# Kernel optimization log

Measured on AMD Instinct MI355X. Metric: run time of the kernel, lower is better.

Reference implementation:

```python
import jax, jax.numpy as jnp
import numpy as np

L = 2        # rnn_layers
H = 512      # hidden size
T_MAX = 20   # text_max_len
V = 10000    # NUM_WORDS
B = 32       # batch
S = 49       # spatial positions (7x7)


def setup_inputs() -> dict:
    key = jax.random.key(0)
    ks = jax.random.split(key, 12)
    w = lambda k, shape: jax.random.normal(k, shape, dtype=jnp.float32) * 0.02
    return {
        "img_channels": jax.random.normal(ks[0], (B, 512, 7, 7), dtype=jnp.float32),
        "pooled": jax.random.normal(ks[1], (B, H), dtype=jnp.float32),
        "embed_table": w(ks[2], (V, H)),
        "Wq": w(ks[3], (H, H)), "bq": jnp.zeros((H,), jnp.float32),
        "Wk": w(ks[4], (S, S)), "bk": jnp.zeros((S,), jnp.float32),
        "Wv": w(ks[5], (S, S)), "bv": jnp.zeros((S,), jnp.float32),
        "Wih": w(ks[6], (L, 4 * H, H)), "Whh": w(ks[7], (L, 4 * H, H)),
        "bih": jnp.zeros((L, 4 * H), jnp.float32), "bhh": jnp.zeros((L, 4 * H), jnp.float32),
        "projW": w(ks[8], (V, H)), "projb": jnp.zeros((V,), jnp.float32),
        "hattW": w(ks[9], (H, 2 * H)), "hattb": jnp.zeros((H,), jnp.float32),
        "sos_idx": 1,
    }


def _lstm_cell(x, h, c, wih, whh, bi, bh):
    # PyTorch gate order: i, f, g, o
    g = x @ wih.T + bi + h @ whh.T + bh
    i, f, gg, o = jnp.split(g, 4, axis=-1)
    c2 = jax.nn.sigmoid(f) * c + jax.nn.sigmoid(i) * jnp.tanh(gg)
    return jax.nn.sigmoid(o) * jnp.tanh(c2), c2


def reference(img_channels, pooled, embed_table, Wq, bq, Wk, bk, Wv, bv,
              Wih, Whh, bih, bhh, projW, projb, hattW, hattb, sos_idx):
    Bsz = img_channels.shape[0]
    chan = img_channels.reshape(Bsz, 512, -1)           # [B,512,49]
    # keys/values are step-invariant: precompute once
    keys = jnp.tanh(chan @ Wk.T + bk)                    # [B,512,49]
    values = jnp.tanh(chan @ Wv.T + bv)                  # [B,512,49]

    emb0 = jnp.broadcast_to(embed_table[sos_idx], (Bsz, H))   # <SOS> embedding
    h0 = jnp.broadcast_to(pooled[None], (L, Bsz, H))
    c0 = h0

    def step(carry, _):
        emb, h, c = carry
        x = emb
        hs, cs = [], []
        for l in range(L):  # small fixed layer count
            hl, cl = _lstm_cell(x, h[l], c[l], Wih[l], Whh[l], bih[l], bhh[l])
            hs.append(hl); cs.append(cl)
            x = hl
        out = x                                          # [B,H] top-layer output
        h = jnp.stack(hs); c = jnp.stack(cs)
        # greedy next-token embedding (no teacher forcing)
        logits = out @ projW.T + projb                   # [B,V]
        emb_next = embed_table[jnp.argmax(logits, axis=-1)]
        # cross-attention gated hidden update (all layers at once)
        q = jnp.tanh(h @ Wq.T + bq)                      # [L,B,H]
        scores = jnp.einsum('lbd,bds->lbs', q, keys) / 7.0
        w = jax.nn.softmax(scores, axis=-1)              # [L,B,49]
        attn = jnp.einsum('lbs,bds->lbd', w, values)     # [L,B,H]
        h = jnp.tanh(jnp.concatenate([attn, h], axis=-1) @ hattW.T + hattb)
        return (emb_next, h, c), out

    _, outs = jax.lax.scan(step, (emb0, h0, c0), None, length=T_MAX - 1)
    pred = jnp.concatenate([emb0[None], outs], axis=0)   # [T,B,H]
    res = jnp.einsum('tbd,vd->bvt', pred, projW) + projb[None, :, None]
    return res                                           # [B,V,T]
```

## Files before the change

kernel.cpp:

```cpp
#include <hip/hip_runtime.h>

namespace {

constexpr int B = 32, H = 512, L = 2, T = 20, V = 10000, S = 49;

__device__ __forceinline__ float sigf(float x) { return 1.0f / (1.0f + expf(-x)); }
__device__ __forceinline__ float dot4(float4 a, float4 b) {
  return a.x*b.x + a.y*b.y + a.z*b.z + a.w*b.w;
}

__global__ __launch_bounds__(256) void kv_kernel(
    const float* __restrict__ chan,
    const float* __restrict__ Wk, const float* __restrict__ bk,
    const float* __restrict__ Wv, const float* __restrict__ bv,
    float* __restrict__ keysT, float* __restrict__ valuesT) {
  __shared__ float ch[64][52];
  __shared__ float wk[49][52], wv[49][52];
  int b = blockIdx.x >> 3, dt = blockIdx.x & 7;
  int tid = threadIdx.x;
  for (int i = tid; i < 49 * 49; i += 256) {
    int s = i / 49, j = i % 49;
    wk[s][j] = Wk[i]; wv[s][j] = Wv[i];
  }
  for (int i = tid; i < 64 * 49; i += 256) {
    int d = i / 49, j = i % 49;
    ch[d][j] = chan[((size_t)b * 512 + dt * 64 + d) * S + j];
  }
  __syncthreads();
  int dl = tid >> 2, sq = tid & 3;
  for (int s = sq; s < S; s += 4) {
    float ak = bk[s], av = bv[s];
    for (int j = 0; j < 49; ++j) {
      float cv = ch[dl][j];
      ak += cv * wk[s][j];
      av += cv * wv[s][j];
    }
    int d = dt * 64 + dl;
    keysT[((size_t)b * S + s) * H + d] = tanhf(ak);
    valuesT[((size_t)b * S + s) * H + d] = tanhf(av);
  }
}

__global__ void init_kernel(const float* __restrict__ pooled,
                            const float* __restrict__ embed,
                            const int* __restrict__ sos,
                            float* __restrict__ emb, float* __restrict__ h,
                            float* __restrict__ c) {
  int idx = blockIdx.x * 256 + threadIdx.x;
  float p = pooled[idx & (B * H - 1)];
  h[idx] = p;
  c[idx] = p;
  if (idx < B * H) emb[idx] = embed[sos[0] * H + (idx & (H - 1))];
}

__global__ __launch_bounds__(256) void lstm_kernel(
    const float* __restrict__ x, const float* __restrict__ hprev,
    const float* __restrict__ cprev,
    const float* __restrict__ Wih, const float* __restrict__ Whh,
    const float* __restrict__ bih, const float* __restrict__ bhh,
    float* __restrict__ hout, float* __restrict__ cout) {
  __shared__ __align__(16) float smem[32 * 512];
  int tid = threadIdx.x;
  int hi = blockIdx.x;
  int ko = tid & 15, rr = (tid >> 4) & 3, bh = tid >> 6;

  {
    const float4* xg = (const float4*)x;
    float4* s4 = (float4*)smem;
    for (int i = tid; i < 4096; i += 256) s4[i] = xg[i];
  }
  __syncthreads();

  float acc[8];
#pragma unroll
  for (int j = 0; j < 8; ++j) acc[j] = 0.f;
  {
    const float* wrow = Wih + ((size_t)rr * H + hi) * H;
    float4 w[8];
#pragma unroll
    for (int kk = 0; kk < 8; ++kk) w[kk] = *(const float4*)&wrow[kk * 64 + ko * 4];
#pragma unroll
    for (int j = 0; j < 8; ++j) {
      const float* xb = smem + (bh * 8 + j) * 512;
#pragma unroll
      for (int kk = 0; kk < 8; ++kk)
        acc[j] += dot4(*(const float4*)&xb[kk * 64 + ko * 4], w[kk]);
    }
  }
  __syncthreads();
  {
    const float4* hg = (const float4*)hprev;
    float4* s4 = (float4*)smem;
    for (int i = tid; i < 4096; i += 256) s4[i] = hg[i];
  }
  __syncthreads();
  {
    const float* wrow = Whh + ((size_t)rr * H + hi) * H;
    float4 w[8];
#pragma unroll
    for (int kk = 0; kk < 8; ++kk) w[kk] = *(const float4*)&wrow[kk * 64 + ko * 4];
#pragma unroll
    for (int j = 0; j < 8; ++j) {
      const float* xb = smem + (bh * 8 + j) * 512;
#pragma unroll
      for (int kk = 0; kk < 8; ++kk)
        acc[j] += dot4(*(const float4*)&xb[kk * 64 + ko * 4], w[kk]);
    }
  }
  __syncthreads();

#pragma unroll
  for (int j = 0; j < 8; ++j) {
    acc[j] += __shfl_xor(acc[j], 1);
    acc[j] += __shfl_xor(acc[j], 2);
    acc[j] += __shfl_xor(acc[j], 4);
    acc[j] += __shfl_xor(acc[j], 8);
  }
  float* gbuf = smem;
  if (ko == 0) {
    float bias = bih[rr * H + hi] + bhh[rr * H + hi];
#pragma unroll
    for (int j = 0; j < 8; ++j) gbuf[rr * 32 + bh * 8 + j] = acc[j] + bias;
  }
  __syncthreads();
  if (tid < 32) {
    int b = tid;
    float gi = gbuf[b], gf = gbuf[32 + b], gg = gbuf[64 + b], go = gbuf[96 + b];
    float c2 = sigf(gf) * cprev[b * H + hi] + sigf(gi) * tanhf(gg);
    hout[b * H + hi] = sigf(go) * tanhf(c2);
    cout[b * H + hi] = c2;
  }
}

__global__ __launch_bounds__(256) void projq_kernel(
    const float* __restrict__ xin,
    const float* __restrict__ projW, const float* __restrict__ projb,
    float* __restrict__ logits, float* __restrict__ ocol, int direct, int tcol,
    const float* __restrict__ hmid_all, const float* __restrict__ Wq,
    const float* __restrict__ bq, float* __restrict__ q) {
  __shared__ __align__(16) float xs[32 * 512];
  int blk = blockIdx.x, tid = threadIdx.x;
  int ko = tid & 15, vl = tid >> 4;

  if (blk < 625) {
    {
      const float4* xg = (const float4*)xin;
      float4* s4 = (float4*)xs;
      for (int i = tid; i < 4096; i += 256) s4[i] = xg[i];
    }
    __syncthreads();
    int v = blk * 16 + vl;
    const float* wrow = projW + (size_t)v * H;
    float4 w[8];
#pragma unroll
    for (int kk = 0; kk < 8; ++kk) w[kk] = *(const float4*)&wrow[kk * 64 + ko * 4];
    float acc[32];
#pragma unroll
    for (int b = 0; b < 32; ++b) acc[b] = 0.f;
    for (int b = 0; b < 32; ++b) {
      const float* xb = xs + b * 512;
#pragma unroll
      for (int kk = 0; kk < 8; ++kk)
        acc[b] += dot4(*(const float4*)&xb[kk * 64 + ko * 4], w[kk]);
    }
#pragma unroll
    for (int b = 0; b < 32; ++b) {
      acc[b] += __shfl_xor(acc[b], 1);
      acc[b] += __shfl_xor(acc[b], 2);
      acc[b] += __shfl_xor(acc[b], 4);
      acc[b] += __shfl_xor(acc[b], 8);
    }
    if (ko == 0) {
      float bias = projb[v];
      for (int b = 0; b < 32; ++b) {
        float r = acc[b] + bias;
        logits[b * V + v] = r;
        if (direct) ocol[((size_t)b * V + v) * T + tcol] = r;
        else        ocol[b * V + v] = r;
      }
    }
  } else {
    int b2 = blk - 625;
    int lg = b2 & 1, jg = b2 >> 1;
    {
      const float4* xg = (const float4*)(hmid_all + lg * 32 * H);
      float4* s4 = (float4*)xs;
      for (int i = tid; i < 4096; i += 256) s4[i] = xg[i];
    }
    __syncthreads();
    int j = jg * 16 + vl;
    const float* wrow = Wq + (size_t)j * H;
    float4 w[8];
#pragma unroll
    for (int kk = 0; kk < 8; ++kk) w[kk] = *(const float4*)&wrow[kk * 64 + ko * 4];
    float acc[32];
#pragma unroll
    for (int b = 0; b < 32; ++b) acc[b] = 0.f;
    for (int b = 0; b < 32; ++b) {
      const float* xb = xs + b * 512;
#pragma unroll
      for (int kk = 0; kk < 8; ++kk)
        acc[b] += dot4(*(const float4*)&xb[kk * 64 + ko * 4], w[kk]);
    }
#pragma unroll
    for (int b = 0; b < 32; ++b) {
      acc[b] += __shfl_xor(acc[b], 1);
      acc[b] += __shfl_xor(acc[b], 2);
      acc[b] += __shfl_xor(acc[b], 4);
      acc[b] += __shfl_xor(acc[b], 8);
    }
    if (ko == 0) {
      float bias = bq[j];
      for (int b = 0; b < 32; ++b)
        q[(lg * 32 + b) * H + j] = tanhf(acc[b] + bias);
    }
  }
}

__global__ __launch_bounds__(256) void sattn_kernel(
    const float* __restrict__ q, const float* __restrict__ keysT,
    const float* __restrict__ valuesT, const float* __restrict__ hmid,
    float* __restrict__ cat) {
  __shared__ __align__(16) float qv[528];
  __shared__ float scl[64];
  __shared__ float wts[64];
  int lb = blockIdx.x, tid = threadIdx.x;
  int b = lb & 31;
  {
    int c0 = tid, c1 = tid + 256;
    qv[(c0 >> 7) * 132 + (c0 & 127)] = q[lb * H + c0];
    qv[(c1 >> 7) * 132 + (c1 & 127)] = q[lb * H + c1];
  }
  __syncthreads();
  int kq = tid & 3, sl = tid >> 2;
  float acc = 0.f;
  if (sl < S) {
    const float* kr = keysT + ((size_t)b * S + sl) * H + kq * 128;
    const float* qr = &qv[kq * 132];
    for (int k = 0; k < 128; k += 4)
      acc += dot4(*(const float4*)&qr[k], *(const float4*)&kr[k]);
  }
  acc += __shfl_xor(acc, 1);
  acc += __shfl_xor(acc, 2);
  if (kq == 0 && sl < S) scl[sl] = acc * (1.0f / 7.0f);
  __syncthreads();
  if (tid < 64) {
    float sc = (tid < S) ? scl[tid] : -3.4e38f;
    float m = sc;
    for (int o = 32; o > 0; o >>= 1) m = fmaxf(m, __shfl_xor(m, o));
    float e = (tid < S) ? expf(sc - m) : 0.f;
    float sum = e;
    for (int o = 32; o > 0; o >>= 1) sum += __shfl_xor(sum, o);
    if (tid < S) wts[tid] = e / sum;
  }
  __syncthreads();
  float acc0 = 0.f, acc1 = 0.f;
  for (int s = 0; s < S; ++s) {
    float w = wts[s];
    const float* vr = valuesT + ((size_t)b * S + s) * H;
    acc0 += w * vr[tid];
    acc1 += w * vr[tid + 256];
  }
  cat[lb * 1024 + tid] = acc0;
  cat[lb * 1024 + tid + 256] = acc1;
  cat[lb * 1024 + 512 + tid] = hmid[lb * H + tid];
  cat[lb * 1024 + 768 + tid] = hmid[lb * H + tid + 256];
}

__global__ __launch_bounds__(256) void hattarg_kernel(
    const float* __restrict__ cat, const float* __restrict__ hattW,
    const float* __restrict__ hattb, float* __restrict__ h,
    const float* __restrict__ logits, const float* __restrict__ embed,
    float* __restrict__ emb) {
  __shared__ __align__(16) float smem[16 * 1024];
  int blk = blockIdx.x, tid = threadIdx.x;
  if (blk < 128) {
    int lbg = blk & 3, jg = blk >> 2;
    {
      const float4* cg = (const float4*)(cat + lbg * 16 * 1024);
      float4* s4 = (float4*)smem;
      for (int i = tid; i < 4096; i += 256) s4[i] = cg[i];
    }
    __syncthreads();
    int ko = tid & 15, jl = tid >> 4;
    int j = jg * 16 + jl;
    const float* wrow = hattW + (size_t)j * 1024;
    float4 w[16];
#pragma unroll
    for (int kk = 0; kk < 16; ++kk) w[kk] = *(const float4*)&wrow[kk * 64 + ko * 4];
    float acc[16];
#pragma unroll
    for (int lb = 0; lb < 16; ++lb) acc[lb] = 0.f;
    for (int lb = 0; lb < 16; ++lb) {
      const float* cb = smem + lb * 1024;
#pragma unroll
      for (int kk = 0; kk < 16; ++kk)
        acc[lb] += dot4(*(const float4*)&cb[kk * 64 + ko * 4], w[kk]);
    }
#pragma unroll
    for (int lb = 0; lb < 16; ++lb) {
      acc[lb] += __shfl_xor(acc[lb], 1);
      acc[lb] += __shfl_xor(acc[lb], 2);
      acc[lb] += __shfl_xor(acc[lb], 4);
      acc[lb] += __shfl_xor(acc[lb], 8);
    }
    if (ko == 0) {
      float bias = hattb[j];
      for (int lb = 0; lb < 16; ++lb)
        h[(lbg * 16 + lb) * H + j] = tanhf(acc[lb] + bias);
    }
  } else {
    int b = blk - 128;
    float* sv = smem;
    int* si = (int*)(smem + 256);
    float best = -3.4e38f;
    int bi = 0x7fffffff;
    for (int it = 0; it < 10; ++it) {
      int v0 = it * 1024 + tid * 4;
      if (v0 < V) {
        float4 lv = *(const float4*)&logits[b * V + v0];
        if (lv.x > best) { best = lv.x; bi = v0; }
        if (lv.y > best) { best = lv.y; bi = v0 + 1; }
        if (lv.z > best) { best = lv.z; bi = v0 + 2; }
        if (lv.w > best) { best = lv.w; bi = v0 + 3; }
      }
    }
    sv[tid] = best; si[tid] = bi;
    __syncthreads();
    for (int st = 128; st > 0; st >>= 1) {
      if (tid < st) {
        float ov = sv[tid + st]; int oi = si[tid + st];
        if (ov > sv[tid] || (ov == sv[tid] && oi < si[tid])) { sv[tid] = ov; si[tid] = oi; }
      }
      __syncthreads();
    }
    int idx = si[0];
    for (int i = tid; i < H; i += 256) emb[b * H + i] = embed[(size_t)idx * H + i];
  }
}

__global__ __launch_bounds__(256) void finalize_kernel(
    const float* __restrict__ slog, float* __restrict__ outp) {
  int idx = blockIdx.x * 256 + threadIdx.x;
  float vals[T];
#pragma unroll
  for (int t = 0; t < T; ++t) vals[t] = slog[(size_t)t * (B * V) + idx];
#pragma unroll
  for (int t = 0; t < T; t += 4)
    *(float4*)&outp[(size_t)idx * T + t] =
        make_float4(vals[t], vals[t + 1], vals[t + 2], vals[t + 3]);
}

}

extern "C" void kernel_launch(void* const* d_in, const int* in_sizes, int n_in,
                              void* d_out, int out_size, void* d_ws, size_t ws_size,
                              hipStream_t stream) {
  const float* chan   = (const float*)d_in[0];
  const float* pooled = (const float*)d_in[1];
  const float* embed  = (const float*)d_in[2];
  const float* Wq     = (const float*)d_in[3];
  const float* bq     = (const float*)d_in[4];
  const float* Wk     = (const float*)d_in[5];
  const float* bk     = (const float*)d_in[6];
  const float* Wv     = (const float*)d_in[7];
  const float* bv     = (const float*)d_in[8];
  const float* Wih    = (const float*)d_in[9];
  const float* Whh    = (const float*)d_in[10];
  const float* bih    = (const float*)d_in[11];
  const float* bhh    = (const float*)d_in[12];
  const float* projW  = (const float*)d_in[13];
  const float* projb  = (const float*)d_in[14];
  const float* hattW  = (const float*)d_in[15];
  const float* hattb  = (const float*)d_in[16];
  const int*   sos    = (const int*)d_in[17];

  float* out = (float*)d_out;
  float* ws  = (float*)d_ws;

  float* keysT   = ws;
  float* valuesT = keysT + B * S * 512;
  float* emb     = valuesT + B * S * 512;
  float* h       = emb + B * H;
  float* c       = h + L * B * H;
  float* hmid    = c + L * B * H;
  float* cat     = hmid + L * B * H;
  float* q       = cat + L * B * 1024;
  float* logits  = q + L * B * H;
  float* slog    = logits + B * V;

  size_t base_floats = (size_t)(slog - ws);
  bool staged = ws_size >= (base_floats + (size_t)T * B * V) * sizeof(float);

  kv_kernel<<<256, 256, 0, stream>>>(chan, Wk, bk, Wv, bv, keysT, valuesT);
  init_kernel<<<(L * B * H) / 256, 256, 0, stream>>>(pooled, embed, sos, emb, h, c);
  {
    float* oc = staged ? slog : out;
    projq_kernel<<<625, 256, 0, stream>>>(emb, projW, projb, logits, oc,
                                          staged ? 0 : 1, 0,
                                          hmid, Wq, bq, q);
  }

  for (int t = 0; t < T - 1; ++t) {
    float* oc = staged ? (slog + (size_t)(t + 1) * B * V) : out;
    lstm_kernel<<<512, 256, 0, stream>>>(emb, h, c, Wih, Whh, bih, bhh, hmid, c);
    lstm_kernel<<<512, 256, 0, stream>>>(hmid, h + B * H, c + B * H,
                                         Wih + 4 * H * H, Whh + 4 * H * H,
                                         bih + 4 * H, bhh + 4 * H,
                                         hmid + B * H, c + B * H);
    projq_kernel<<<689, 256, 0, stream>>>(hmid + B * H, projW, projb, logits, oc,
                                          staged ? 0 : 1, t + 1,
                                          hmid, Wq, bq, q);
    sattn_kernel<<<L * B, 256, 0, stream>>>(q, keysT, valuesT, hmid, cat);
    hattarg_kernel<<<160, 256, 0, stream>>>(cat, hattW, hattb, h,
                                            logits, embed, emb);
  }

  if (staged) finalize_kernel<<<(B * V) / 256, 256, 0, stream>>>(slog, out);
}
```

Before: 1.984 ms.

## Replace per-step kernel launches with a single persistent kernel using grid barriers

Fuses the whole decode loop (kv precompute, init, LSTM layers, projection, query, attention, argmax, hidden update, finalize) into one persistent kernel of 256 blocks that synchronise through an atomic-counter grid barrier. This removes roughly a hundred kernel launches and their launch gaps, and regroups stages so argmax runs alongside attention. It relies on all 256 blocks being co-resident. The barrier has a spin-count escape that could silently break correctness if it times out, and the old multi-kernel path is kept only as a fallback when workspace is too small.

Result: slower. 6.021 ms (+203.5%).

```diff
diff --git a/kernel.cpp b/kernel.cpp
--- a/kernel.cpp
+++ b/kernel.cpp
@@ -3,11 +3,383 @@
 namespace {
 
 constexpr int B = 32, H = 512, L = 2, T = 20, V = 10000, S = 49;
+constexpr int NB = 256, NT = 512;
 
 __device__ __forceinline__ float sigf(float x) { return 1.0f / (1.0f + expf(-x)); }
 __device__ __forceinline__ float dot4(float4 a, float4 b) {
   return a.x*b.x + a.y*b.y + a.z*b.z + a.w*b.w;
 }
+
+struct KParams {
+  const float *chan, *pooled, *embed, *Wq, *bq, *Wk, *bk, *Wv, *bv,
+              *Wih, *Whh, *bih, *bhh, *projW, *projb, *hattW, *hattb;
+  const int* sos;
+  float* out;
+  float* ws;
+  int* cnt;
+};
+
+__device__ __forceinline__ void gsync(int* cnt, int target) {
+  __syncthreads();
+  if (threadIdx.x == 0) {
+    __threadfence();
+    atomicAdd(cnt, 1);
+    unsigned spins = 0;
+    while (atomicAdd(cnt, 0) < target) {
+      __builtin_amdgcn_s_sleep(8);
+      if (++spins > (1u << 20)) break;
+    }
+    __threadfence();
+  }
+  __syncthreads();
+}
+
+
+__device__ __forceinline__ void stage64k(const float* __restrict__ src,
+                                         float* smem, int tid) {
+  const float4* g = (const float4*)src;
+  float4* s4 = (float4*)smem;
+  for (int i = tid; i < 4096; i += NT) s4[i] = g[i];
+}
+
+__device__ __forceinline__ void lstm_do(
+    const float* __restrict__ x, const float* __restrict__ hp,
+    float* __restrict__ cp, const float* __restrict__ Wih,
+    const float* __restrict__ Whh, const float* __restrict__ bih,
+    const float* __restrict__ bhh, float* __restrict__ ho,
+    float* smem, int blk, int tid) {
+  int tl = tid & 255, hh = tid >> 8;
+  int ko = tl & 15, rr = (tl >> 4) & 3, bh = tl >> 6;
+  int hi = blk * 2 + hh;
+  stage64k(x, smem, tid);
+  __syncthreads();
+  float acc[8];
+#pragma unroll
+  for (int j = 0; j < 8; ++j) acc[j] = 0.f;
+  {
+    const float* wrow = Wih + ((size_t)rr * H + hi) * H;
+    float4 w[8];
+#pragma unroll
+    for (int kk = 0; kk < 8; ++kk) w[kk] = *(const float4*)&wrow[kk * 64 + ko * 4];
+#pragma unroll
+    for (int j = 0; j < 8; ++j) {
+      const float* xb = smem + (bh * 8 + j) * 512;
+#pragma unroll
+      for (int kk = 0; kk < 8; ++kk)
+        acc[j] += dot4(*(const float4*)&xb[kk * 64 + ko * 4], w[kk]);
+    }
+  }
+  __syncthreads();
+  stage64k(hp, smem, tid);
+  __syncthreads();
+  {
+    const float* wrow = Whh + ((size_t)rr * H + hi) * H;
+    float4 w[8];
+#pragma unroll
+    for (int kk = 0; kk < 8; ++kk) w[kk] = *(const float4*)&wrow[kk * 64 + ko * 4];
+#pragma unroll
+    for (int j = 0; j < 8; ++j) {
+      const float* xb = smem + (bh * 8 + j) * 512;
+#pragma unroll
+      for (int kk = 0; kk < 8; ++kk)
+        acc[j] += dot4(*(const float4*)&xb[kk * 64 + ko * 4], w[kk]);
+    }
+  }
+  __syncthreads();
+#pragma unroll
+  for (int j = 0; j < 8; ++j) {
+    acc[j] += __shfl_xor(acc[j], 1);
+    acc[j] += __shfl_xor(acc[j], 2);
+    acc[j] += __shfl_xor(acc[j], 4);
+    acc[j] += __shfl_xor(acc[j], 8);
+  }
+  float* gbuf = smem;
+  if (ko == 0) {
+    float bias = bih[rr * H + hi] + bhh[rr * H + hi];
+#pragma unroll
+    for (int j = 0; j < 8; ++j) gbuf[hh * 128 + rr * 32 + bh * 8 + j] = acc[j] + bias;
+  }
+  __syncthreads();
+  if (tid < 64) {
+    int hs = tid >> 5, b = tid & 31;
+    int hi2 = blk * 2 + hs;
+    const float* gb = gbuf + hs * 128;
+    float gi = gb[b], gf = gb[32 + b], gg = gb[64 + b], go = gb[96 + b];
+    float c2 = sigf(gf) * cp[b * H + hi2] + sigf(gi) * tanhf(gg);
+    ho[b * H + hi2] = sigf(go) * tanhf(c2);
+    cp[b * H + hi2] = c2;
+  }
+}
+
+__device__ __forceinline__ void proj_do(
+    const float* __restrict__ x, float* __restrict__ dst,
+    const float* __restrict__ projW, const float* __restrict__ projb,
+    float* smem, int blk, int tid) {
+  stage64k(x, smem, tid);
+  __syncthreads();
+  int ko = tid & 15, vl = tid >> 4;
+  for (int chunk = blk; chunk < 313; chunk += NB) {
+    int v = chunk * 32 + vl;
+    if (v < V) {
+      const float* wrow = projW + (size_t)v * H;
+      float4 w[8];
+#pragma unroll
+      for (int kk = 0; kk < 8; ++kk) w[kk] = *(const float4*)&wrow[kk * 64 + ko * 4];
+      float acc[32];
+#pragma unroll
+      for (int b = 0; b < 32; ++b) acc[b] = 0.f;
+      for (int b = 0; b < 32; ++b) {
+        const float* xb = smem + b * 512;
+#pragma unroll
+        for (int kk = 0; kk < 8; ++kk)
+          acc[b] += dot4(*(const float4*)&xb[kk * 64 + ko * 4], w[kk]);
+      }
+#pragma unroll
+      for (int b = 0; b < 32; ++b) {
+        acc[b] += __shfl_xor(acc[b], 1);
+        acc[b] += __shfl_xor(acc[b], 2);
+        acc[b] += __shfl_xor(acc[b], 4);
+        acc[b] += __shfl_xor(acc[b], 8);
+      }
+      if (ko == 0) {
+        float bias = projb[v];
+        for (int b = 0; b < 32; ++b) dst[(size_t)b * V + v] = acc[b] + bias;
+      }
+    }
+  }
+}
+
+__device__ __forceinline__ void q_do(
+    const float* __restrict__ hmid, const float* __restrict__ Wq,
+    const float* __restrict__ bq, float* __restrict__ q,
+    float* smem, int u, int tid) {
+  int lg = u & 1, jg = u >> 1;
+  __syncthreads();
+  stage64k(hmid + (size_t)lg * B * H, smem, tid);
+  __syncthreads();
+  int ko = tid & 15, jl = tid >> 4;
+  int j = jg * 32 + jl;
+  const float* wrow = Wq + (size_t)j * H;
+  float4 w[8];
+#pragma unroll
+  for (int kk = 0; kk < 8; ++kk) w[kk] = *(const float4*)&wrow[kk * 64 + ko * 4];
+  float acc[32];
+#pragma unroll
+  for (int b = 0; b < 32; ++b) acc[b] = 0.f;
+  for (int b = 0; b < 32; ++b) {
+    const float* xb = smem + b * 512;
+#pragma unroll
+    for (int kk = 0; kk < 8; ++kk)
+      acc[b] += dot4(*(const float4*)&xb[kk * 64 + ko * 4], w[kk]);
+  }
+#pragma unroll
+  for (int b = 0; b < 32; ++b) {
+    acc[b] += __shfl_xor(acc[b], 1);
+    acc[b] += __shfl_xor(acc[b], 2);
+    acc[b] += __shfl_xor(acc[b], 4);
+    acc[b] += __shfl_xor(acc[b], 8);
+  }
+  if (ko == 0) {
+    float bias = bq[j];
+    for (int b = 0; b < 32; ++b)
+      q[(size_t)(lg * 32 + b) * H + j] = tanhf(acc[b] + bias);
+  }
+}
+
+__device__ __forceinline__ void sattn_do(
+    const float* __restrict__ q, const float* __restrict__ keysT,
+    const float* __restrict__ valuesT, const float* __restrict__ hmid,
+    float* __restrict__ cat, float* smem, int lb, int tid) {
+  float* qv = smem;
+  float* scl = smem + 544;
+  float* wts = smem + 608;
+  int b = lb & 31;
+  qv[(tid >> 7) * 132 + (tid & 127)] = q[(size_t)lb * H + tid];
+  __syncthreads();
+  int kq = tid & 3, sl = tid >> 2;
+  float acc = 0.f;
+  if (sl < S) {
+    const float* kr = keysT + ((size_t)b * S + sl) * H + kq * 128;
+    const float* qr = &qv[kq * 132];
+    for (int k = 0; k < 128; k += 4)
+      acc += dot4(*(const float4*)&qr[k], *(const float4*)&kr[k]);
+  }
+  acc += __shfl_xor(acc, 1);
+  acc += __shfl_xor(acc, 2);
+  if (kq == 0 && sl < S) scl[sl] = acc * (1.0f / 7.0f);
+  __syncthreads();
+  if (tid < 64) {
+    float sc = (tid < S) ? scl[tid] : -3.4e38f;
+    float m = sc;
+    for (int o = 32; o > 0; o >>= 1) m = fmaxf(m, __shfl_xor(m, o));
+    float e = (tid < S) ? expf(sc - m) : 0.f;
+    float sum = e;
+    for (int o = 32; o > 0; o >>= 1) sum += __shfl_xor(sum, o);
+    if (tid < S) wts[tid] = e / sum;
+  }
+  __syncthreads();
+  float a0 = 0.f;
+  for (int s = 0; s < S; ++s)
+    a0 += wts[s] * valuesT[((size_t)b * S + s) * H + tid];
+  cat[(size_t)lb * 1024 + tid] = a0;
+  cat[(size_t)lb * 1024 + 512 + tid] = hmid[(size_t)lb * H + tid];
+}
+
+__device__ __forceinline__ void argmax_do(
+    const float* __restrict__ lgts, const float* __restrict__ embed,
+    float* __restrict__ emb, float* smem, int b, int tid) {
+  float* sv = smem;
+  int* si = (int*)(smem + 512);
+  float best = -3.4e38f;
+  int bi = 0x7fffffff;
+  for (int it = 0; it < 5; ++it) {
+    int v0 = it * 2048 + tid * 4;
+    if (v0 < V) {
+      float4 lv = *(const float4*)&lgts[(size_t)b * V + v0];
+      if (lv.x > best) { best = lv.x; bi = v0; }
+      if (lv.y > best) { best = lv.y; bi = v0 + 1; }
+      if (lv.z > best) { best = lv.z; bi = v0 + 2; }
+      if (lv.w > best) { best = lv.w; bi = v0 + 3; }
+    }
+  }
+  sv[tid] = best; si[tid] = bi;
+  __syncthreads();
+  for (int st = 256; st > 0; st >>= 1) {
+    if (tid < st) {
+      float ov = sv[tid + st]; int oi = si[tid + st];
+      if (ov > sv[tid] || (ov == sv[tid] && oi < si[tid])) { sv[tid] = ov; si[tid] = oi; }
+    }
+    __syncthreads();
+  }
+  int idx = si[0];
+  emb[(size_t)b * H + tid] = embed[(size_t)idx * H + tid];
+}
+
+__device__ __forceinline__ void hatt_do(
+    const float* __restrict__ cat, const float* __restrict__ hattW,
+    const float* __restrict__ hattb, float* __restrict__ h,
+    float* smem, int blk, int tid) {
+  int lbg = blk & 3, jg = blk >> 2;
+  stage64k(cat + (size_t)lbg * 16 * 1024, smem, tid);
+  __syncthreads();
+  int ko = tid & 15, jl = tid >> 4;
+  int j = jg * 32 + jl;
+  const float* wrow = hattW + (size_t)j * 1024;
+  float4 w[16];
+#pragma unroll
+  for (int kk = 0; kk < 16; ++kk) w[kk] = *(const float4*)&wrow[kk * 64 + ko * 4];
+  float acc[16];
+#pragma unroll
+  for (int lb = 0; lb < 16; ++lb) acc[lb] = 0.f;
+  for (int lb = 0; lb < 16; ++lb) {
+    const float* cb = smem + lb * 1024;
+#pragma unroll
+    for (int kk = 0; kk < 16; ++kk)
+      acc[lb] += dot4(*(const float4*)&cb[kk * 64 + ko * 4], w[kk]);
+  }
+#pragma unroll
+  for (int lb = 0; lb < 16; ++lb) {
+    acc[lb] += __shfl_xor(acc[lb], 1);
+    acc[lb] += __shfl_xor(acc[lb], 2);
+    acc[lb] += __shfl_xor(acc[lb], 4);
+    acc[lb] += __shfl_xor(acc[lb], 8);
+  }
+  if (ko == 0) {
+    float bias = hattb[j];
+    for (int lb = 0; lb < 16; ++lb)
+      h[(size_t)(lbg * 16 + lb) * H + j] = tanhf(acc[lb] + bias);
+  }
+}
+
+__global__ __launch_bounds__(NT, 4) void persist(KParams p) {
+  __shared__ __align__(16) float smem[16384];
+  const int blk = blockIdx.x, tid = threadIdx.x;
+  int* cnt = p.cnt;
+  int ep = 0;
+
+  float* keysT   = p.ws;
+  float* valuesT = keysT + B * S * H;
+  float* emb     = valuesT + B * S * H;
+  float* h       = emb + B * H;
+  float* c       = h + L * B * H;
+  float* hmid    = c + L * B * H;
+  float* cat     = hmid + L * B * H;
+  float* q       = cat + L * B * 1024;
+  float* logits  = q + L * B * H;
+  float* slog    = logits + B * V;
+
+  {
+    float* ch = smem;
+    float* wk = smem + 64 * 52;
+    float* wv = wk + 49 * 52;
+    int b = blk >> 3, dt = blk & 7;
+    for (int i = tid; i < 49 * 49; i += NT) {
+      int s = i / 49, j = i % 49;
+      wk[s * 52 + j] = p.Wk[i]; wv[s * 52 + j] = p.Wv[i];
+    }
+    for (int i = tid; i < 64 * 49; i += NT) {
+      int d = i / 49, j = i % 49;
+      ch[d * 52 + j] = p.chan[((size_t)b * 512 + dt * 64 + d) * S + j];
+    }
+    __syncthreads();
+    int dl = tid >> 3, sq = tid & 7;
+    for (int s = sq; s < S; s += 8) {
+      float ak = p.bk[s], av = p.bv[s];
+      for (int j = 0; j < 49; ++j) {
+        float cv = ch[dl * 52 + j];
+        ak += cv * wk[s * 52 + j];
+        av += cv * wv[s * 52 + j];
+      }
+      int d = dt * 64 + dl;
+      keysT[((size_t)b * S + s) * H + d] = tanhf(ak);
+      valuesT[((size_t)b * S + s) * H + d] = tanhf(av);
+    }
+    int idx = blk * NT + tid;
+    if (idx < L * B * H) {
+      float pv = p.pooled[idx & (B * H - 1)];
+      h[idx] = pv; c[idx] = pv;
+      if (idx < B * H) emb[idx] = p.embed[(size_t)p.sos[0] * H + (idx & (H - 1))];
+    }
+  }
+  gsync(cnt, (++ep) * NB);
+
+  proj_do(emb, slog, p.projW, p.projb, smem, blk, tid);
+  gsync(cnt, (++ep) * NB);
+
+#pragma unroll 1
+  for (int t = 0; t < T - 1; ++t) {
+    lstm_do(emb, h, c, p.Wih, p.Whh, p.bih, p.bhh, hmid, smem, blk, tid);
+    gsync(cnt, (++ep) * NB);
+    lstm_do(hmid, h + B * H, c + B * H, p.Wih + 4 * H * H, p.Whh + 4 * H * H,
+            p.bih + 4 * H, p.bhh + 4 * H, hmid + B * H, smem, blk, tid);
+    gsync(cnt, (++ep) * NB);
+    proj_do(hmid + B * H, slog + (size_t)(t + 1) * B * V, p.projW, p.projb,
+            smem, blk, tid);
+    if (t < T - 2 && blk >= 57 && blk < 89)
+      q_do(hmid, p.Wq, p.bq, q, smem, blk - 57, tid);
+    gsync(cnt, (++ep) * NB);
+    if (t < T - 2) {
+      if (blk < 64)
+        sattn_do(q, keysT, valuesT, hmid, cat, smem, blk, tid);
+      else if (blk < 96)
+        argmax_do(slog + (size_t)(t + 1) * B * V, p.embed, emb, smem, blk - 64, tid);
+      gsync(cnt, (++ep) * NB);
+      if (blk < 64) hatt_do(cat, p.hattW, p.hattb, h, smem, blk, tid);
+      gsync(cnt, (++ep) * NB);
+    }
+  }
+
+  for (int i = blk * NT + tid; i < B * V; i += NB * NT) {
+    float vals[T];
+#pragma unroll
+    for (int t = 0; t < T; ++t) vals[t] = slog[(size_t)t * (B * V) + i];
+#pragma unroll
+    for (int t = 0; t < T; t += 4)
+      *(float4*)&p.out[(size_t)i * T + t] =
+          make_float4(vals[t], vals[t + 1], vals[t + 2], vals[t + 3]);
+  }
+}
+
 
 __global__ __launch_bounds__(256) void kv_kernel(
     const float* __restrict__ chan,
@@ -63,14 +435,12 @@
   int tid = threadIdx.x;
   int hi = blockIdx.x;
   int ko = tid & 15, rr = (tid >> 4) & 3, bh = tid >> 6;
-
   {
     const float4* xg = (const float4*)x;
     float4* s4 = (float4*)smem;
     for (int i = tid; i < 4096; i += 256) s4[i] = xg[i];
   }
   __syncthreads();
-
   float acc[8];
 #pragma unroll
   for (int j = 0; j < 8; ++j) acc[j] = 0.f;
@@ -108,7 +478,6 @@
     }
   }
   __syncthreads();
-
 #pragma unroll
   for (int j = 0; j < 8; ++j) {
     acc[j] += __shfl_xor(acc[j], 1);
@@ -141,7 +510,6 @@
   __shared__ __align__(16) float xs[32 * 512];
   int blk = blockIdx.x, tid = threadIdx.x;
   int ko = tid & 15, vl = tid >> 4;
-
   if (blk < 625) {
     {
       const float4* xg = (const float4*)xin;
@@ -277,9 +645,9 @@
   if (blk < 128) {
     int lbg = blk & 3, jg = blk >> 2;
     {
-      const float4* cg = (const float4*)(cat + lbg * 16 * 1024);
+      const float4* cg2 = (const float4*)(cat + lbg * 16 * 1024);
       float4* s4 = (float4*)smem;
-      for (int i = tid; i < 4096; i += 256) s4[i] = cg[i];
+      for (int i = tid; i < 4096; i += 256) s4[i] = cg2[i];
     }
     __syncthreads();
     int ko = tid & 15, jl = tid >> 4;
@@ -356,6 +724,7 @@
 extern "C" void kernel_launch(void* const* d_in, const int* in_sizes, int n_in,
                               void* d_out, int out_size, void* d_ws, size_t ws_size,
                               hipStream_t stream) {
+  (void)in_sizes; (void)n_in; (void)out_size;
   const float* chan   = (const float*)d_in[0];
   const float* pooled = (const float*)d_in[1];
   const float* embed  = (const float*)d_in[2];
@@ -376,7 +745,8 @@
   const int*   sos    = (const int*)d_in[17];
 
   float* out = (float*)d_out;
-  float* ws  = (float*)d_ws;
+  int*   cnt = (int*)d_ws;
+  float* ws  = (float*)d_ws + 64;
 
   float* keysT   = ws;
   float* valuesT = keysT + B * S * 512;
@@ -389,7 +759,19 @@
   float* logits  = q + L * B * H;
   float* slog    = logits + B * V;
 
-  size_t base_floats = (size_t)(slog - ws);
+  size_t need_floats = 64 + (size_t)(slog - ws) + (size_t)T * B * V;
+  bool fits = ws_size >= need_floats * sizeof(float);
+
+  if (fits) {
+    hipMemsetAsync(d_ws, 0, 256, stream);
+    KParams p = {chan, pooled, embed, Wq, bq, Wk, bk, Wv, bv,
+                 Wih, Whh, bih, bhh, projW, projb, hattW, hattb,
+                 sos, out, ws, cnt};
+    persist<<<NB, NT, 0, stream>>>(p);
+    return;
+  }
+
+  size_t base_floats = (size_t)(slog - ws) + 64;
   bool staged = ws_size >= (base_floats + (size_t)T * B * V) * sizeof(float);
 
   kv_kernel<<<256, 256, 0, stream>>>(chan, Wk, bk, Wv, bv, keysT, valuesT);
@@ -400,7 +782,6 @@
                                           staged ? 0 : 1, 0,
                                           hmid, Wq, bq, q);
   }
-
   for (int t = 0; t < T - 1; ++t) {
     float* oc = staged ? (slog + (size_t)(t + 1) * B * V) : out;
     lstm_kernel<<<512, 256, 0, stream>>>(emb, h, c, Wih, Whh, bih, bhh, hmid, c);
@@ -415,6 +796,5 @@
     hattarg_kernel<<<160, 256, 0, stream>>>(cat, hattW, hattb, h,
                                             logits, embed, emb);
   }
-
   if (staged) finalize_kernel<<<(B * V) / 256, 256, 0, stream>>>(slog, out);
 }
```

## Fuse setup kernels, merge query projection into attention, drop redundant final-step work

Applied to the files above, without the earlier changes.

When the staging workspace is available, this adds a single setup kernel that builds keys/values, initial states and the step-0 logits. The step-0 projection is computed once for the shared SOS embedding and broadcast across the batch. A new projsat kernel computes the vocab projection into the staged slice and lets each attention block compute its own query row before doing attention, which removes a separate launch. The argmax now reads from the staged logits, and the last step skips the attention and hidden-update work whose results are never used. Together these cut launches and redundant compute. The cost is that each attention block recomputes a full 512x512 GEMV row-set serially, so the query step loses parallelism.

Result: slower. 2.035 ms (+2.6%).

```diff
diff --git a/kernel.cpp b/kernel.cpp
--- a/kernel.cpp
+++ b/kernel.cpp
@@ -8,6 +8,344 @@
 __device__ __forceinline__ float dot4(float4 a, float4 b) {
   return a.x*b.x + a.y*b.y + a.z*b.z + a.w*b.w;
 }
+
+__global__ __launch_bounds__(256) void setup_kernel(
+    const float* __restrict__ chan,
+    const float* __restrict__ Wk, const float* __restrict__ bk,
+    const float* __restrict__ Wv, const float* __restrict__ bv,
+    float* __restrict__ keysT, float* __restrict__ valuesT,
+    const float* __restrict__ pooled, const float* __restrict__ embed,
+    const int* __restrict__ sos,
+    float* __restrict__ emb, float* __restrict__ h, float* __restrict__ c,
+    const float* __restrict__ projW, const float* __restrict__ projb,
+    float* __restrict__ slog0) {
+  __shared__ __align__(16) float smem[8448];
+  int blk = blockIdx.x, tid = threadIdx.x;
+  if (blk < 256) {
+    float* ch = smem;
+    float* wk = smem + 64 * 52;
+    float* wv = wk + 49 * 52;
+    int b = blk >> 3, dt = blk & 7;
+    for (int i = tid; i < 49 * 49; i += 256) {
+      int s = i / 49, j = i % 49;
+      wk[s * 52 + j] = Wk[i]; wv[s * 52 + j] = Wv[i];
+    }
+    for (int i = tid; i < 64 * 49; i += 256) {
+      int d = i / 49, j = i % 49;
+      ch[d * 52 + j] = chan[((size_t)b * 512 + dt * 64 + d) * S + j];
+    }
+    __syncthreads();
+    int dl = tid >> 2, sq = tid & 3;
+    for (int s = sq; s < S; s += 4) {
+      float ak = bk[s], av = bv[s];
+      for (int j = 0; j < 49; ++j) {
+        float cv = ch[dl * 52 + j];
+        ak += cv * wk[s * 52 + j];
+        av += cv * wv[s * 52 + j];
+      }
+      int d = dt * 64 + dl;
+      keysT[((size_t)b * S + s) * H + d] = tanhf(ak);
+      valuesT[((size_t)b * S + s) * H + d] = tanhf(av);
+    }
+  } else if (blk < 384) {
+    int idx = (blk - 256) * 256 + tid;
+    float p = pooled[idx & (B * H - 1)];
+    h[idx] = p;
+    c[idx] = p;
+    if (idx < B * H) emb[idx] = embed[(size_t)sos[0] * H + (idx & (H - 1))];
+  } else {
+    float* es = smem;
+    es[tid] = embed[(size_t)sos[0] * H + tid];
+    es[tid + 256] = embed[(size_t)sos[0] * H + tid + 256];
+    __syncthreads();
+    int ko = tid & 15, vl = tid >> 4;
+    int v = (blk - 384) * 16 + vl;
+    const float* wrow = projW + (size_t)v * H;
+    float4 w[8];
+#pragma unroll
+    for (int kk = 0; kk < 8; ++kk) w[kk] = *(const float4*)&wrow[kk * 64 + ko * 4];
+    float acc = 0.f;
+#pragma unroll
+    for (int kk = 0; kk < 8; ++kk)
+      acc += dot4(*(const float4*)&es[kk * 64 + ko * 4], w[kk]);
+    acc += __shfl_xor(acc, 1);
+    acc += __shfl_xor(acc, 2);
+    acc += __shfl_xor(acc, 4);
+    acc += __shfl_xor(acc, 8);
+    if (ko == 0) {
+      float r = acc + projb[v];
+      for (int b = 0; b < 32; ++b) slog0[(size_t)b * V + v] = r;
+    }
+  }
+}
+
+__global__ __launch_bounds__(256) void lstm_kernel(
+    const float* __restrict__ x, const float* __restrict__ hprev,
+    const float* __restrict__ cprev,
+    const float* __restrict__ Wih, const float* __restrict__ Whh,
+    const float* __restrict__ bih, const float* __restrict__ bhh,
+    float* __restrict__ hout, float* __restrict__ cout) {
+  __shared__ __align__(16) float smem[32 * 512];
+  int tid = threadIdx.x;
+  int hi = blockIdx.x;
+  int ko = tid & 15, rr = (tid >> 4) & 3, bh = tid >> 6;
+  {
+    const float4* xg = (const float4*)x;
+    float4* s4 = (float4*)smem;
+    for (int i = tid; i < 4096; i += 256) s4[i] = xg[i];
+  }
+  __syncthreads();
+  float acc[8];
+#pragma unroll
+  for (int j = 0; j < 8; ++j) acc[j] = 0.f;
+  {
+    const float* wrow = Wih + ((size_t)rr * H + hi) * H;
+    float4 w[8];
+#pragma unroll
+    for (int kk = 0; kk < 8; ++kk) w[kk] = *(const float4*)&wrow[kk * 64 + ko * 4];
+#pragma unroll
+    for (int j = 0; j < 8; ++j) {
+      const float* xb = smem + (bh * 8 + j) * 512;
+#pragma unroll
+      for (int kk = 0; kk < 8; ++kk)
+        acc[j] += dot4(*(const float4*)&xb[kk * 64 + ko * 4], w[kk]);
+    }
+  }
+  __syncthreads();
+  {
+    const float4* hg = (const float4*)hprev;
+    float4* s4 = (float4*)smem;
+    for (int i = tid; i < 4096; i += 256) s4[i] = hg[i];
+  }
+  __syncthreads();
+  {
+    const float* wrow = Whh + ((size_t)rr * H + hi) * H;
+    float4 w[8];
+#pragma unroll
+    for (int kk = 0; kk < 8; ++kk) w[kk] = *(const float4*)&wrow[kk * 64 + ko * 4];
+#pragma unroll
+    for (int j = 0; j < 8; ++j) {
+      const float* xb = smem + (bh * 8 + j) * 512;
+#pragma unroll
+      for (int kk = 0; kk < 8; ++kk)
+        acc[j] += dot4(*(const float4*)&xb[kk * 64 + ko * 4], w[kk]);
+    }
+  }
+  __syncthreads();
+#pragma unroll
+  for (int j = 0; j < 8; ++j) {
+    acc[j] += __shfl_xor(acc[j], 1);
+    acc[j] += __shfl_xor(acc[j], 2);
+    acc[j] += __shfl_xor(acc[j], 4);
+    acc[j] += __shfl_xor(acc[j], 8);
+  }
+  float* gbuf = smem;
+  if (ko == 0) {
+    float bias = bih[rr * H + hi] + bhh[rr * H + hi];
+#pragma unroll
+    for (int j = 0; j < 8; ++j) gbuf[rr * 32 + bh * 8 + j] = acc[j] + bias;
+  }
+  __syncthreads();
+  if (tid < 32) {
+    int b = tid;
+    float gi = gbuf[b], gf = gbuf[32 + b], gg = gbuf[64 + b], go = gbuf[96 + b];
+    float c2 = sigf(gf) * cprev[b * H + hi] + sigf(gi) * tanhf(gg);
+    hout[b * H + hi] = sigf(go) * tanhf(c2);
+    cout[b * H + hi] = c2;
+  }
+}
+
+__global__ __launch_bounds__(256) void projsat_kernel(
+    const float* __restrict__ hmid_all,
+    const float* __restrict__ projW, const float* __restrict__ projb,
+    const float* __restrict__ Wq, const float* __restrict__ bq,
+    const float* __restrict__ keysT, const float* __restrict__ valuesT,
+    float* __restrict__ dst, float* __restrict__ cat) {
+  __shared__ __align__(16) float smem[32 * 512];
+  int blk = blockIdx.x, tid = threadIdx.x;
+  if (blk < 625) {
+    const float* xin = hmid_all + B * H;
+    {
+      const float4* xg = (const float4*)xin;
+      float4* s4 = (float4*)smem;
+      for (int i = tid; i < 4096; i += 256) s4[i] = xg[i];
+    }
+    __syncthreads();
+    int ko = tid & 15, vl = tid >> 4;
+    int v = blk * 16 + vl;
+    const float* wrow = projW + (size_t)v * H;
+    float4 w[8];
+#pragma unroll
+    for (int kk = 0; kk < 8; ++kk) w[kk] = *(const float4*)&wrow[kk * 64 + ko * 4];
+    float acc[32];
+#pragma unroll
+    for (int b = 0; b < 32; ++b) acc[b] = 0.f;
+    for (int b = 0; b < 32; ++b) {
+      const float* xb = smem + b * 512;
+#pragma unroll
+      for (int kk = 0; kk < 8; ++kk)
+        acc[b] += dot4(*(const float4*)&xb[kk * 64 + ko * 4], w[kk]);
+    }
+#pragma unroll
+    for (int b = 0; b < 32; ++b) {
+      acc[b] += __shfl_xor(acc[b], 1);
+      acc[b] += __shfl_xor(acc[b], 2);
+      acc[b] += __shfl_xor(acc[b], 4);
+      acc[b] += __shfl_xor(acc[b], 8);
+    }
+    if (ko == 0) {
+      float bias = projb[v];
+      for (int b = 0; b < 32; ++b) dst[(size_t)b * V + v] = acc[b] + bias;
+    }
+  } else {
+    int lb = blk - 625;
+    int b = lb & 31, lg = lb >> 5;
+    float* hr  = smem;
+    float* qv  = smem + 512;
+    float* scl = smem + 1040;
+    float* wts = smem + 1104;
+    const float* hrow = hmid_all + (size_t)lg * B * H + (size_t)b * H;
+    hr[tid] = hrow[tid];
+    hr[tid + 256] = hrow[tid + 256];
+    __syncthreads();
+    int ko = tid & 15, vl = tid >> 4;
+    for (int jg = 0; jg < 32; ++jg) {
+      int j = jg * 16 + vl;
+      const float* wrow = Wq + (size_t)j * H;
+      float4 w[8];
+#pragma unroll
+      for (int kk = 0; kk < 8; ++kk) w[kk] = *(const float4*)&wrow[kk * 64 + ko * 4];
+      float acc = 0.f;
+#pragma unroll
+      for (int kk = 0; kk < 8; ++kk)
+        acc += dot4(*(const float4*)&hr[kk * 64 + ko * 4], w[kk]);
+      acc += __shfl_xor(acc, 1);
+      acc += __shfl_xor(acc, 2);
+      acc += __shfl_xor(acc, 4);
+      acc += __shfl_xor(acc, 8);
+      if (ko == 0) qv[(j >> 7) * 132 + (j & 127)] = tanhf(acc + bq[j]);
+    }
+    __syncthreads();
+    int kq = tid & 3, sl = tid >> 2;
+    float acc = 0.f;
+    if (sl < S) {
+      const float* kr = keysT + ((size_t)b * S + sl) * H + kq * 128;
+      const float* qr = &qv[kq * 132];
+      for (int k = 0; k < 128; k += 4)
+        acc += dot4(*(const float4*)&qr[k], *(const float4*)&kr[k]);
+    }
+    acc += __shfl_xor(acc, 1);
+    acc += __shfl_xor(acc, 2);
+    if (kq == 0 && sl < S) scl[sl] = acc * (1.0f / 7.0f);
+    __syncthreads();
+    if (tid < 64) {
+      float sc = (tid < S) ? scl[tid] : -3.4e38f;
+      float m = sc;
+      for (int o = 32; o > 0; o >>= 1) m = fmaxf(m, __shfl_xor(m, o));
+      float e = (tid < S) ? expf(sc - m) : 0.f;
+      float sum = e;
+      for (int o = 32; o > 0; o >>= 1) sum += __shfl_xor(sum, o);
+      if (tid < S) wts[tid] = e / sum;
+    }
+    __syncthreads();
+    float acc0 = 0.f, acc1 = 0.f;
+    for (int s = 0; s < S; ++s) {
+      float w = wts[s];
+      const float* vr = valuesT + ((size_t)b * S + s) * H;
+      acc0 += w * vr[tid];
+      acc1 += w * vr[tid + 256];
+    }
+    cat[lb * 1024 + tid] = acc0;
+    cat[lb * 1024 + tid + 256] = acc1;
+    cat[lb * 1024 + 512 + tid] = hmid_all[lb * H + tid];
+    cat[lb * 1024 + 768 + tid] = hmid_all[lb * H + tid + 256];
+  }
+}
+
+__global__ __launch_bounds__(256) void hattarg_kernel(
+    const float* __restrict__ cat, const float* __restrict__ hattW,
+    const float* __restrict__ hattb, float* __restrict__ h,
+    const float* __restrict__ logits, const float* __restrict__ embed,
+    float* __restrict__ emb) {
+  __shared__ __align__(16) float smem[16 * 1024];
+  int blk = blockIdx.x, tid = threadIdx.x;
+  if (blk < 128) {
+    int lbg = blk & 3, jg = blk >> 2;
+    {
+      const float4* cg2 = (const float4*)(cat + lbg * 16 * 1024);
+      float4* s4 = (float4*)smem;
+      for (int i = tid; i < 4096; i += 256) s4[i] = cg2[i];
+    }
+    __syncthreads();
+    int ko = tid & 15, jl = tid >> 4;
+    int j = jg * 16 + jl;
+    const float* wrow = hattW + (size_t)j * 1024;
+    float4 w[16];
+#pragma unroll
+    for (int kk = 0; kk < 16; ++kk) w[kk] = *(const float4*)&wrow[kk * 64 + ko * 4];
+    float acc[16];
+#pragma unroll
+    for (int lb = 0; lb < 16; ++lb) acc[lb] = 0.f;
+    for (int lb = 0; lb < 16; ++lb) {
+      const float* cb = smem + lb * 1024;
+#pragma unroll
+      for (int kk = 0; kk < 16; ++kk)
+        acc[lb] += dot4(*(const float4*)&cb[kk * 64 + ko * 4], w[kk]);
+    }
+#pragma unroll
+    for (int lb = 0; lb < 16; ++lb) {
+      acc[lb] += __shfl_xor(acc[lb], 1);
+      acc[lb] += __shfl_xor(acc[lb], 2);
+      acc[lb] += __shfl_xor(acc[lb], 4);
+      acc[lb] += __shfl_xor(acc[lb], 8);
+    }
+    if (ko == 0) {
+      float bias = hattb[j];
+      for (int lb = 0; lb < 16; ++lb)
+        h[(lbg * 16 + lb) * H + j] = tanhf(acc[lb] + bias);
+    }
+  } else {
+    int b = blk - 128;
+    float* sv = smem;
+    int* si = (int*)(smem + 256);
+    float best = -3.4e38f;
+    int bi = 0x7fffffff;
+    for (int it = 0; it < 10; ++it) {
+      int v0 = it * 1024 + tid * 4;
+      if (v0 < V) {
+        float4 lv = *(const float4*)&logits[(size_t)b * V + v0];
+        if (lv.x > best) { best = lv.x; bi = v0; }
+        if (lv.y > best) { best = lv.y; bi = v0 + 1; }
+        if (lv.z > best) { best = lv.z; bi = v0 + 2; }
+        if (lv.w > best) { best = lv.w; bi = v0 + 3; }
+      }
+    }
+    sv[tid] = best; si[tid] = bi;
+    __syncthreads();
+    for (int st = 128; st > 0; st >>= 1) {
+      if (tid < st) {
+        float ov = sv[tid + st]; int oi = si[tid + st];
+        if (ov > sv[tid] || (ov == sv[tid] && oi < si[tid])) { sv[tid] = ov; si[tid] = oi; }
+      }
+      __syncthreads();
+    }
+    int idx = si[0];
+    for (int i = tid; i < H; i += 256) emb[b * H + i] = embed[(size_t)idx * H + i];
+  }
+}
+
+__global__ __launch_bounds__(256) void finalize_kernel(
+    const float* __restrict__ slog, float* __restrict__ outp) {
+  int idx = blockIdx.x * 256 + threadIdx.x;
+  float vals[T];
+#pragma unroll
+  for (int t = 0; t < T; ++t) vals[t] = slog[(size_t)t * (B * V) + idx];
+#pragma unroll
+  for (int t = 0; t < T; t += 4)
+    *(float4*)&outp[(size_t)idx * T + t] =
+        make_float4(vals[t], vals[t + 1], vals[t + 2], vals[t + 3]);
+}
+
 
 __global__ __launch_bounds__(256) void kv_kernel(
     const float* __restrict__ chan,
@@ -53,85 +391,6 @@
   if (idx < B * H) emb[idx] = embed[sos[0] * H + (idx & (H - 1))];
 }
 
-__global__ __launch_bounds__(256) void lstm_kernel(
-    const float* __restrict__ x, const float* __restrict__ hprev,
-    const float* __restrict__ cprev,
-    const float* __restrict__ Wih, const float* __restrict__ Whh,
-    const float* __restrict__ bih, const float* __restrict__ bhh,
-    float* __restrict__ hout, float* __restrict__ cout) {
-  __shared__ __align__(16) float smem[32 * 512];
-  int tid = threadIdx.x;
-  int hi = blockIdx.x;
-  int ko = tid & 15, rr = (tid >> 4) & 3, bh = tid >> 6;
-
-  {
-    const float4* xg = (const float4*)x;
-    float4* s4 = (float4*)smem;
-    for (int i = tid; i < 4096; i += 256) s4[i] = xg[i];
-  }
-  __syncthreads();
-
-  float acc[8];
-#pragma unroll
-  for (int j = 0; j < 8; ++j) acc[j] = 0.f;
-  {
-    const float* wrow = Wih + ((size_t)rr * H + hi) * H;
-    float4 w[8];
-#pragma unroll
-    for (int kk = 0; kk < 8; ++kk) w[kk] = *(const float4*)&wrow[kk * 64 + ko * 4];
-#pragma unroll
-    for (int j = 0; j < 8; ++j) {
-      const float* xb = smem + (bh * 8 + j) * 512;
-#pragma unroll
-      for (int kk = 0; kk < 8; ++kk)
-        acc[j] += dot4(*(const float4*)&xb[kk * 64 + ko * 4], w[kk]);
-    }
-  }
-  __syncthreads();
-  {
-    const float4* hg = (const float4*)hprev;
-    float4* s4 = (float4*)smem;
-    for (int i = tid; i < 4096; i += 256) s4[i] = hg[i];
-  }
-  __syncthreads();
-  {
-    const float* wrow = Whh + ((size_t)rr * H + hi) * H;
-    float4 w[8];
-#pragma unroll
-    for (int kk = 0; kk < 8; ++kk) w[kk] = *(const float4*)&wrow[kk * 64 + ko * 4];
-#pragma unroll
-    for (int j = 0; j < 8; ++j) {
-      const float* xb = smem + (bh * 8 + j) * 512;
-#pragma unroll
-      for (int kk = 0; kk < 8; ++kk)
-        acc[j] += dot4(*(const float4*)&xb[kk * 64 + ko * 4], w[kk]);
-    }
-  }
-  __syncthreads();
-
-#pragma unroll
-  for (int j = 0; j < 8; ++j) {
-    acc[j] += __shfl_xor(acc[j], 1);
-    acc[j] += __shfl_xor(acc[j], 2);
-    acc[j] += __shfl_xor(acc[j], 4);
-    acc[j] += __shfl_xor(acc[j], 8);
-  }
-  float* gbuf = smem;
-  if (ko == 0) {
-    float bias = bih[rr * H + hi] + bhh[rr * H + hi];
-#pragma unroll
-    for (int j = 0; j < 8; ++j) gbuf[rr * 32 + bh * 8 + j] = acc[j] + bias;
-  }
-  __syncthreads();
-  if (tid < 32) {
-    int b = tid;
-    float gi = gbuf[b], gf = gbuf[32 + b], gg = gbuf[64 + b], go = gbuf[96 + b];
-    float c2 = sigf(gf) * cprev[b * H + hi] + sigf(gi) * tanhf(gg);
-    hout[b * H + hi] = sigf(go) * tanhf(c2);
-    cout[b * H + hi] = c2;
-  }
-}
-
 __global__ __launch_bounds__(256) void projq_kernel(
     const float* __restrict__ xin,
     const float* __restrict__ projW, const float* __restrict__ projb,
@@ -141,7 +400,6 @@
   __shared__ __align__(16) float xs[32 * 512];
   int blk = blockIdx.x, tid = threadIdx.x;
   int ko = tid & 15, vl = tid >> 4;
-
   if (blk < 625) {
     {
       const float4* xg = (const float4*)xin;
@@ -267,95 +525,12 @@
   cat[lb * 1024 + 768 + tid] = hmid[lb * H + tid + 256];
 }
 
-__global__ __launch_bounds__(256) void hattarg_kernel(
-    const float* __restrict__ cat, const float* __restrict__ hattW,
-    const float* __restrict__ hattb, float* __restrict__ h,
-    const float* __restrict__ logits, const float* __restrict__ embed,
-    float* __restrict__ emb) {
-  __shared__ __align__(16) float smem[16 * 1024];
-  int blk = blockIdx.x, tid = threadIdx.x;
-  if (blk < 128) {
-    int lbg = blk & 3, jg = blk >> 2;
-    {
-      const float4* cg = (const float4*)(cat + lbg * 16 * 1024);
-      float4* s4 = (float4*)smem;
-      for (int i = tid; i < 4096; i += 256) s4[i] = cg[i];
-    }
-    __syncthreads();
-    int ko = tid & 15, jl = tid >> 4;
-    int j = jg * 16 + jl;
-    const float* wrow = hattW + (size_t)j * 1024;
-    float4 w[16];
-#pragma unroll
-    for (int kk = 0; kk < 16; ++kk) w[kk] = *(const float4*)&wrow[kk * 64 + ko * 4];
-    float acc[16];
-#pragma unroll
-    for (int lb = 0; lb < 16; ++lb) acc[lb] = 0.f;
-    for (int lb = 0; lb < 16; ++lb) {
-      const float* cb = smem + lb * 1024;
-#pragma unroll
-      for (int kk = 0; kk < 16; ++kk)
-        acc[lb] += dot4(*(const float4*)&cb[kk * 64 + ko * 4], w[kk]);
-    }
-#pragma unroll
-    for (int lb = 0; lb < 16; ++lb) {
-      acc[lb] += __shfl_xor(acc[lb], 1);
-      acc[lb] += __shfl_xor(acc[lb], 2);
-      acc[lb] += __shfl_xor(acc[lb], 4);
-      acc[lb] += __shfl_xor(acc[lb], 8);
-    }
-    if (ko == 0) {
-      float bias = hattb[j];
-      for (int lb = 0; lb < 16; ++lb)
-        h[(lbg * 16 + lb) * H + j] = tanhf(acc[lb] + bias);
-    }
-  } else {
-    int b = blk - 128;
-    float* sv = smem;
-    int* si = (int*)(smem + 256);
-    float best = -3.4e38f;
-    int bi = 0x7fffffff;
-    for (int it = 0; it < 10; ++it) {
-      int v0 = it * 1024 + tid * 4;
-      if (v0 < V) {
-        float4 lv = *(const float4*)&logits[b * V + v0];
-        if (lv.x > best) { best = lv.x; bi = v0; }
-        if (lv.y > best) { best = lv.y; bi = v0 + 1; }
-        if (lv.z > best) { best = lv.z; bi = v0 + 2; }
-        if (lv.w > best) { best = lv.w; bi = v0 + 3; }
-      }
-    }
-    sv[tid] = best; si[tid] = bi;
-    __syncthreads();
-    for (int st = 128; st > 0; st >>= 1) {
-      if (tid < st) {
-        float ov = sv[tid + st]; int oi = si[tid + st];
-        if (ov > sv[tid] || (ov == sv[tid] && oi < si[tid])) { sv[tid] = ov; si[tid] = oi; }
-      }
-      __syncthreads();
-    }
-    int idx = si[0];
-    for (int i = tid; i < H; i += 256) emb[b * H + i] = embed[(size_t)idx * H + i];
-  }
-}
-
-__global__ __launch_bounds__(256) void finalize_kernel(
-    const float* __restrict__ slog, float* __restrict__ outp) {
-  int idx = blockIdx.x * 256 + threadIdx.x;
-  float vals[T];
-#pragma unroll
-  for (int t = 0; t < T; ++t) vals[t] = slog[(size_t)t * (B * V) + idx];
-#pragma unroll
-  for (int t = 0; t < T; t += 4)
-    *(float4*)&outp[(size_t)idx * T + t] =
-        make_float4(vals[t], vals[t + 1], vals[t + 2], vals[t + 3]);
-}
-
 }
 
 extern "C" void kernel_launch(void* const* d_in, const int* in_sizes, int n_in,
                               void* d_out, int out_size, void* d_ws, size_t ws_size,
                               hipStream_t stream) {
+  (void)in_sizes; (void)n_in; (void)out_size;
   const float* chan   = (const float*)d_in[0];
   const float* pooled = (const float*)d_in[1];
   const float* embed  = (const float*)d_in[2];
@@ -392,29 +567,42 @@
   size_t base_floats = (size_t)(slog - ws);
   bool staged = ws_size >= (base_floats + (size_t)T * B * V) * sizeof(float);
 
+  if (staged) {
+    setup_kernel<<<1009, 256, 0, stream>>>(chan, Wk, bk, Wv, bv, keysT, valuesT,
+                                           pooled, embed, sos, emb, h, c,
+                                           projW, projb, slog);
+    for (int t = 0; t < T - 1; ++t) {
+      float* dst = slog + (size_t)(t + 1) * B * V;
+      lstm_kernel<<<512, 256, 0, stream>>>(emb, h, c, Wih, Whh, bih, bhh, hmid, c);
+      lstm_kernel<<<512, 256, 0, stream>>>(hmid, h + B * H, c + B * H,
+                                           Wih + 4 * H * H, Whh + 4 * H * H,
+                                           bih + 4 * H, bhh + 4 * H,
+                                           hmid + B * H, c + B * H);
+      bool last = (t == T - 2);
+      projsat_kernel<<<last ? 625 : 689, 256, 0, stream>>>(
+          hmid, projW, projb, Wq, bq, keysT, valuesT, dst, cat);
+      if (!last)
+        hattarg_kernel<<<160, 256, 0, stream>>>(cat, hattW, hattb, h,
+                                                dst, embed, emb);
+    }
+    finalize_kernel<<<(B * V) / 256, 256, 0, stream>>>(slog, out);
+    return;
+  }
+
   kv_kernel<<<256, 256, 0, stream>>>(chan, Wk, bk, Wv, bv, keysT, valuesT);
   init_kernel<<<(L * B * H) / 256, 256, 0, stream>>>(pooled, embed, sos, emb, h, c);
-  {
-    float* oc = staged ? slog : out;
-    projq_kernel<<<625, 256, 0, stream>>>(emb, projW, projb, logits, oc,
-                                          staged ? 0 : 1, 0,
-                                          hmid, Wq, bq, q);
-  }
-
+  projq_kernel<<<625, 256, 0, stream>>>(emb, projW, projb, logits, out,
+                                        1, 0, hmid, Wq, bq, q);
   for (int t = 0; t < T - 1; ++t) {
-    float* oc = staged ? (slog + (size_t)(t + 1) * B * V) : out;
     lstm_kernel<<<512, 256, 0, stream>>>(emb, h, c, Wih, Whh, bih, bhh, hmid, c);
     lstm_kernel<<<512, 256, 0, stream>>>(hmid, h + B * H, c + B * H,
                                          Wih + 4 * H * H, Whh + 4 * H * H,
                                          bih + 4 * H, bhh + 4 * H,
                                          hmid + B * H, c + B * H);
-    projq_kernel<<<689, 256, 0, stream>>>(hmid + B * H, projW, projb, logits, oc,
-                                          staged ? 0 : 1, t + 1,
-                                          hmid, Wq, bq, q);
+    projq_kernel<<<689, 256, 0, stream>>>(hmid + B * H, projW, projb, logits, out,
+                                          1, t + 1, hmid, Wq, bq, q);
     sattn_kernel<<<L * B, 256, 0, stream>>>(q, keysT, valuesT, hmid, cat);
     hattarg_kernel<<<160, 256, 0, stream>>>(cat, hattW, hattb, h,
                                             logits, embed, emb);
   }
-
-  if (staged) finalize_kernel<<<(B * V) / 256, 256, 0, stream>>>(slog, out);
-}
+}
```
